# Optimization experiments

Measured on AMD Instinct MI355X. Metric: run time of the kernel, lower is better.

The kernel has to match this reference:

```python
import jax, jax.numpy as jnp
import numpy as np

SIM_TIME = 3
ALPHA = 0.9      # membrane decay
RHO = 0.985      # threshold-adaptation decay
BETA_A = 1.8     # adaptation coupling
TH = 1.0         # base threshold
SURR_SCALE = 0.3 # surrogate gradient scale

@jax.custom_vjp
def spike(v):
    return (v > 0.0).astype(v.dtype)

def _spike_fwd(v):
    return spike(v), v

def _spike_bwd(v, g):
    # triangular surrogate gradient
    return (g * SURR_SCALE * jnp.maximum(0.0, 1.0 - jnp.abs(v)),)

spike.defvjp(_spike_fwd, _spike_bwd)

def setup_inputs() -> dict:
    key = jax.random.key(0)
    ks = jax.random.split(key, 6)
    T, B, nin, npre, nad, npost, nout = 32, 128, 512, 1024, 1024, 1024, 256
    s = lambda fan_in: 1.0 / np.sqrt(fan_in)
    return {
        "inp": jax.random.normal(ks[0], (T, B, nin), dtype=jnp.float32),
        "W_pre": jax.random.normal(ks[1], (npre, nin + nad), dtype=jnp.float32) * s(nin + nad),
        "b_pre": jnp.zeros((npre,), jnp.float32),
        "W_ad": jax.random.normal(ks[2], (nad, npre), dtype=jnp.float32) * s(npre),
        "b_ad": jnp.zeros((nad,), jnp.float32),
        "W_post": jax.random.normal(ks[3], (npost, nin + nad), dtype=jnp.float32) * s(nin + nad),
        "b_post": jnp.zeros((npost,), jnp.float32),
        "W_out": jax.random.normal(ks[4], (nout, npost), dtype=jnp.float32) * s(npost),
        "b_out": jnp.zeros((nout,), jnp.float32),
    }

def _rsnn_forward(inp, W_pre, b_pre, W_ad, b_ad, W_post, b_post, W_out, b_out):
    T, B, _ = inp.shape
    nad = W_ad.shape[0]
    npre = W_pre.shape[0]
    npost = W_post.shape[0]
    z = lambda n: jnp.zeros((B, n), inp.dtype)
    # state: (adaptive spikes, v_pre, v_adapt, b_adapt, v_post)
    init = (z(nad), z(npre), z(nad), z(nad), z(npost))

    def step_t(state, inp_t):
        spikes, v_pre, v_a, b_a, v_post = state
        o = None
        for _ in range(SIM_TIME):  # fixed small inner simulation loop
            x = jnp.concatenate([inp_t, spikes], axis=1)            # [B, nin+nad]
            v_pre = ALPHA * v_pre + x @ W_pre.T + b_pre
            s_pre = spike(v_pre - TH)
            v_pre = v_pre - s_pre * TH                               # soft reset
            v_a = ALPHA * v_a + s_pre @ W_ad.T + b_ad
            th_eff = TH + BETA_A * b_a                               # adaptive threshold
            s_a = spike(v_a - th_eff)
            v_a = v_a - s_a * th_eff
            b_a = RHO * b_a + s_a
            spikes = s_a
            x2 = jnp.concatenate([inp_t, s_a], axis=1)
            v_post = ALPHA * v_post + x2 @ W_post.T + b_post
            s_post = spike(v_post - TH)
            v_post = v_post - s_post * TH
            o = s_post @ W_out.T + b_out                             # [B, nout]
        return (spikes, v_pre, v_a, b_a, v_post), o

    final_state, output = jax.lax.scan(step_t, init, inp)            # output [T, B, nout]
    return output, final_state[0]

def reference(inp, W_pre, b_pre, W_ad, b_ad, W_post, b_post, W_out, b_out):
    return _rsnn_forward(inp, W_pre, b_pre, W_ad, b_ad, W_post, b_post, W_out, b_out)
```

## Files before the change

kernel.cpp:

```cpp
#include <hip/hip_runtime.h>

#pragma clang fp contract(off)

typedef unsigned long long u64;
typedef unsigned int u32;

#define ALPHA  0.9f
#define RHO    0.985f
#define BETA_A 1.8f
#define TH     1.0f
#define CAP    (1 << 24)

__global__ __launch_bounds__(256) void transpose_k(const float* __restrict__ src,
                                                   float* __restrict__ dst,
                                                   int R, int C) {
    __shared__ float tile[32][33];
    const int c0 = blockIdx.x * 32;
    const int r0 = blockIdx.y * 32;
    const int tx = threadIdx.x, ty = threadIdx.y;
#pragma unroll
    for (int i = 0; i < 4; ++i)
        tile[ty + i * 8][tx] = src[(r0 + ty + i * 8) * C + c0 + tx];
    __syncthreads();
#pragma unroll
    for (int i = 0; i < 4; ++i)
        dst[(c0 + ty + i * 8) * R + r0 + tx] = tile[tx][ty + i * 8];
}

__global__ __launch_bounds__(256) void ip_gemm2(const float* __restrict__ inp,
                                                const float* __restrict__ Wt_a,
                                                const float* __restrict__ bias_a,
                                                float* __restrict__ out_a,
                                                const float* __restrict__ Wt_b,
                                                const float* __restrict__ bias_b,
                                                float* __restrict__ out_b) {
    __shared__ __align__(16) float s_in[512 * 20];
    const int tid   = threadIdx.x;
    const int chunk = blockIdx.x;
    const int rbase = blockIdx.y * 16;

    for (int idx = tid; idx < 16 * 512; idx += 256) {
        const int r = idx >> 9, k = idx & 511;
        s_in[k * 20 + r] = inp[(rbase + r) * 512 + k];
    }
    __syncthreads();

    const int n = chunk * 256 + tid;
    float acca[16], accb[16];
#pragma unroll
    for (int r = 0; r < 16; ++r) { acca[r] = 0.f; accb[r] = 0.f; }

    for (int k = 0; k < 512; ++k) {
        const float wa = Wt_a[k * 1024 + n];
        const float wb = Wt_b[k * 1024 + n];
        const float4* p = (const float4*)(s_in + k * 20);
        const float4 x0 = p[0], x1 = p[1], x2 = p[2], x3 = p[3];
        acca[0]  = fmaf(x0.x, wa, acca[0]);  accb[0]  = fmaf(x0.x, wb, accb[0]);
        acca[1]  = fmaf(x0.y, wa, acca[1]);  accb[1]  = fmaf(x0.y, wb, accb[1]);
        acca[2]  = fmaf(x0.z, wa, acca[2]);  accb[2]  = fmaf(x0.z, wb, accb[2]);
        acca[3]  = fmaf(x0.w, wa, acca[3]);  accb[3]  = fmaf(x0.w, wb, accb[3]);
        acca[4]  = fmaf(x1.x, wa, acca[4]);  accb[4]  = fmaf(x1.x, wb, accb[4]);
        acca[5]  = fmaf(x1.y, wa, acca[5]);  accb[5]  = fmaf(x1.y, wb, accb[5]);
        acca[6]  = fmaf(x1.z, wa, acca[6]);  accb[6]  = fmaf(x1.z, wb, accb[6]);
        acca[7]  = fmaf(x1.w, wa, acca[7]);  accb[7]  = fmaf(x1.w, wb, accb[7]);
        acca[8]  = fmaf(x2.x, wa, acca[8]);  accb[8]  = fmaf(x2.x, wb, accb[8]);
        acca[9]  = fmaf(x2.y, wa, acca[9]);  accb[9]  = fmaf(x2.y, wb, accb[9]);
        acca[10] = fmaf(x2.z, wa, acca[10]); accb[10] = fmaf(x2.z, wb, accb[10]);
        acca[11] = fmaf(x2.w, wa, acca[11]); accb[11] = fmaf(x2.w, wb, accb[11]);
        acca[12] = fmaf(x3.x, wa, acca[12]); accb[12] = fmaf(x3.x, wb, accb[12]);
        acca[13] = fmaf(x3.y, wa, acca[13]); accb[13] = fmaf(x3.y, wb, accb[13]);
        acca[14] = fmaf(x3.z, wa, acca[14]); accb[14] = fmaf(x3.z, wb, accb[14]);
        acca[15] = fmaf(x3.w, wa, acca[15]); accb[15] = fmaf(x3.w, wb, accb[15]);
    }
    const float bna = bias_a[n];
    const float bnb = bias_b[n];
#pragma unroll
    for (int r = 0; r < 16; ++r) {
        out_a[(rbase + r) * 1024 + n] = acca[r] + bna;
        out_b[(rbase + r) * 1024 + n] = accb[r] + bnb;
    }
}

__device__ __forceinline__ u64 ld_u64(const u64* p) {
    return __hip_atomic_load(p, __ATOMIC_RELAXED, __HIP_MEMORY_SCOPE_AGENT);
}
__device__ __forceinline__ void st_u64(u64* p, u64 v) {
    __hip_atomic_store(p, v, __ATOMIC_RELAXED, __HIP_MEMORY_SCOPE_AGENT);
}
__device__ __forceinline__ u64 ld_lds(const u64* p) {
    return __hip_atomic_load(p, __ATOMIC_RELAXED, __HIP_MEMORY_SCOPE_WORKGROUP);
}
__device__ __forceinline__ void st_lds(u64* p, u64 v) {
    __hip_atomic_store(p, v, __ATOMIC_RELAXED, __HIP_MEMORY_SCOPE_WORKGROUP);
}
__device__ __forceinline__ int ld_seq(const int* p) {
    return __hip_atomic_load(p, __ATOMIC_ACQUIRE, __HIP_MEMORY_SCOPE_WORKGROUP);
}
__device__ __forceinline__ void st_seq(int* p, int v) {
    __hip_atomic_store(p, v, __ATOMIC_RELEASE, __HIP_MEMORY_SCOPE_WORKGROUP);
}

__device__ __forceinline__ float gatherseg(const char* __restrict__ Wb,
                                           const int* __restrict__ list,
                                           int i0, int i1, int colB) {
    float a0 = 0.f, a1 = 0.f, a2 = 0.f, a3 = 0.f;
    int i = i0;
    for (; i + 4 <= i1; i += 4) {
        const int4 j = *(const int4*)(list + i);
        a0 += *(const float*)(Wb + (u32)(j.x + colB));
        a1 += *(const float*)(Wb + (u32)(j.y + colB));
        a2 += *(const float*)(Wb + (u32)(j.z + colB));
        a3 += *(const float*)(Wb + (u32)(j.w + colB));
    }
    for (; i < i1; ++i) a0 += *(const float*)(Wb + (u32)(list[i] + colB));
    return (a0 + a1) + (a2 + a3);
}

__device__ __forceinline__ void gather2seg(const char* __restrict__ Wc,
                                           const char* __restrict__ Wa,
                                           const int* __restrict__ list,
                                           int cnt, int colB,
                                           float& accC, float& accA) {
    float c0 = 0.f, c1 = 0.f, c2 = 0.f, c3 = 0.f;
    float a0 = 0.f, a1 = 0.f, a2 = 0.f, a3 = 0.f;
    int i = 0;
    for (; i + 4 <= cnt; i += 4) {
        const int4 j = *(const int4*)(list + i);
        c0 += *(const float*)(Wc + (u32)(j.x + colB));
        a0 += *(const float*)(Wa + (u32)(j.x + colB));
        c1 += *(const float*)(Wc + (u32)(j.y + colB));
        a1 += *(const float*)(Wa + (u32)(j.y + colB));
        c2 += *(const float*)(Wc + (u32)(j.z + colB));
        a2 += *(const float*)(Wa + (u32)(j.z + colB));
        c3 += *(const float*)(Wc + (u32)(j.w + colB));
        a3 += *(const float*)(Wa + (u32)(j.w + colB));
    }
    for (; i < cnt; ++i) {
        const u32 off = (u32)(list[i] + colB);
        c0 += *(const float*)(Wc + off);
        a0 += *(const float*)(Wa + off);
    }
    accC = (c0 + c1) + (c2 + c3);
    accA = (a0 + a1) + (a2 + a3);
}

__device__ __forceinline__ float gather_idx(const float* __restrict__ W,
                                            const int* __restrict__ list, int cnt, int col) {
    float a0 = 0.f, a1 = 0.f, a2 = 0.f, a3 = 0.f;
    int i = 0;
    for (; i + 4 <= cnt; i += 4) {
        const int4 j = *(const int4*)(list + i);
        a0 += W[j.x * 256 + col];
        a1 += W[j.y * 256 + col];
        a2 += W[j.z * 256 + col];
        a3 += W[j.w * 256 + col];
    }
    for (; i < cnt; ++i) a0 += W[list[i] * 256 + col];
    return (a0 + a1) + (a2 + a3);
}

__global__ __launch_bounds__(640) void rsnn_nb(
    const float* __restrict__ Wt_pre,
    const float* __restrict__ Wt_ad,
    const float* __restrict__ Wt_post,
    const float* __restrict__ IP_pre,
    const float* __restrict__ IP_post,
    const float* __restrict__ b_ad_p,
    u64* __restrict__ lines,
    u64* __restrict__ spkO,
    float* __restrict__ out)
{
    const int tid  = threadIdx.x;
    const int bid  = blockIdx.x;
    const int x    = bid & 7;
    const int g    = bid >> 3;
    const int s    = x >> 1;
    const int p    = g * 2 + (x & 1);
    const int wid  = tid >> 6;
    const int lane = tid & 63;
    const u64 M32  = 0xffffffffull;

    __shared__ __align__(16) int listP[2][1024];
    __shared__ __align__(16) int listS[2][1024];
    __shared__ u64 ltag[2][2][2][8];
    __shared__ int seqP[2], seqS[2], cntP[2], cntS[2];

    if (tid < 64) ((u64*)ltag)[tid] = 0;
    if (tid < 2) { seqP[tid] = 0; seqS[tid] = 0; }
    __syncthreads();

    const char* WadB    = (const char*)Wt_ad;
    const char* WpreAB  = (const char*)(Wt_pre  + 512 * 1024);
    const char* WpostAB = (const char*)(Wt_post + 512 * 1024);

    if (wid < 8) {
        const int bi   = wid >> 2;
        const int q    = wid & 3;
        const int b    = 2 * p + bi;
        const int col  = s * 256 + q * 64 + lane;
        const int colB = col * 4;

        float v_pre = 0.f, v_a = 0.f, ba = 0.f, v_post = 0.f, accA = 0.f;
        bool  sa = false;
        const float bad = b_ad_p[col];
        float ipre = 0.f, ipost = 0.f;

        for (int e = 1; e <= 96; ++e) {
            const int par = e & 1;
            const u64 tag = ((u64)e) << 32;
            if ((e - 1) % 3 == 0) {
                const int t = (e - 1) / 3;
                ipre  = IP_pre [(t * 128 + b) * 1024 + col];
                ipost = IP_post[(t * 128 + b) * 1024 + col];
            }
            u64* gl0 = lines + ((b * 2 + par) * 2 + 0) * 32;
            u64* gl1 = lines + ((b * 2 + par) * 2 + 1) * 32;

            v_pre = ALPHA * v_pre + ipre + accA;
            float d = v_pre - TH;
            const bool sp = d > 0.f;
            if (sp) v_pre = d;
            {
                const u64 m = __ballot(sp);
                if (lane == 0) {
                    st_u64(&gl0[s * 8 + 2 * q],     tag | (m & M32));
                    st_u64(&gl0[s * 8 + 2 * q + 1], tag | (m >> 32));
                    st_lds(&ltag[bi][par][0][2 * q],     tag | (m & M32));
                    st_lds(&ltag[bi][par][0][2 * q + 1], tag | (m >> 32));
                }
            }
            {
                int gd = 0;
                while (ld_seq(&seqP[bi]) < e && ++gd < CAP) {}
            }
            const float accB = gatherseg(WadB, listP[bi], 0, cntP[bi], colB);
            v_a = ALPHA * v_a + accB + bad;
            const float th = TH + BETA_A * ba;
            d = v_a - th;
            sa = d > 0.f;
            if (sa) v_a = d;
            ba = RHO * ba + (sa ? 1.f : 0.f);
            {
                const u64 m = __ballot(sa);
                if (lane == 0) {
                    st_u64(&gl1[s * 8 + 2 * q],     tag | (m & M32));
                    st_u64(&gl1[s * 8 + 2 * q + 1], tag | (m >> 32));
                    st_lds(&ltag[bi][par][1][2 * q],     tag | (m & M32));
                    st_lds(&ltag[bi][par][1][2 * q + 1], tag | (m >> 32));
                }
            }
            {
                int gd = 0;
                while (ld_seq(&seqS[bi]) < e && ++gd < CAP) {}
            }
            float accC;
            gather2seg(WpostAB, WpreAB, listS[bi], cntS[bi], colB, accC, accA);
            v_post = ALPHA * v_post + ipost + accC;
            d = v_post - TH;
            const bool spost = d > 0.f;
            if (spost) v_post = d;
            if (e % 3 == 0) {
                const u64 m = __ballot(spost);
                if (lane == 0)
                    st_u64(&spkO[(((e - 1) / 3) * 128 + b) * 16 + s * 4 + q], m);
            }
            if (e == 96)
                out[32 * 128 * 256 + b * 1024 + col] = sa ? 1.f : 0.f;
        }
    } else {
        const int bi = wid - 8;
        const int b  = 2 * p + bi;
        const bool act = lane < 32;
        const int sl = lane >> 3, h = lane & 7;
        const int jbase = (sl * 256 + h * 32) << 12;

        for (int e = 1; e <= 96; ++e) {
            const int par = e & 1;
            const u64* gl0 = lines + ((b * 2 + par) * 2 + 0) * 32;
            const u64* gl1 = lines + ((b * 2 + par) * 2 + 1) * 32;

            u32 bits = 0;
            if (act) {
                u64 v; int gd = 0;
                if (sl == s) {
                    do { v = ld_lds(&ltag[bi][par][0][h]); }
                    while ((v >> 32) != (u64)e && ++gd < CAP);
                } else {
                    do { v = ld_u64(&gl0[lane]); }
                    while ((v >> 32) != (u64)e && ++gd < CAP);
                }
                bits = (u32)v;
            }
            {
                const int pc = __popc(bits);
                int incl = pc;
#pragma unroll
                for (int dlt = 1; dlt < 32; dlt <<= 1) {
                    const int v = __shfl_up(incl, dlt, 64);
                    if (lane >= dlt && lane < 32) incl += v;
                }
                int base = incl - pc;
                u32 m = bits;
                while (m) {
                    const int bt = __builtin_ctz(m);
                    m &= m - 1;
                    listP[bi][base++] = jbase + (bt << 12);
                }
                if (lane == 31) { cntP[bi] = incl; st_seq(&seqP[bi], e); }
            }

            bits = 0;
            if (act) {
                u64 v; int gd = 0;
                if (sl == s) {
                    do { v = ld_lds(&ltag[bi][par][1][h]); }
                    while ((v >> 32) != (u64)e && ++gd < CAP);
                } else {
                    do { v = ld_u64(&gl1[lane]); }
                    while ((v >> 32) != (u64)e && ++gd < CAP);
                }
                bits = (u32)v;
            }
            {
                const int pc = __popc(bits);
                int incl = pc;
#pragma unroll
                for (int dlt = 1; dlt < 32; dlt <<= 1) {
                    const int v = __shfl_up(incl, dlt, 64);
                    if (lane >= dlt && lane < 32) incl += v;
                }
                int base = incl - pc;
                u32 m = bits;
                while (m) {
                    const int bt = __builtin_ctz(m);
                    m &= m - 1;
                    listS[bi][base++] = jbase + (bt << 12);
                }
                if (lane == 31) { cntS[bi] = incl; st_seq(&seqS[bi], e); }
            }
        }
    }
}

__global__ __launch_bounds__(256) void out_gemm(const float* __restrict__ Wt_out,
                                                const float* __restrict__ b_out,
                                                const u64* __restrict__ spkO,
                                                float* __restrict__ out) {
    __shared__ u64 bmp[16];
    __shared__ int pc[16];
    __shared__ __align__(16) int list[1024];
    const int r = blockIdx.x, tid = threadIdx.x;
    if (tid < 16) {
        const u64 m = ld_u64(&spkO[r * 16 + tid]);
        bmp[tid] = m;
        pc[tid]  = __popcll(m);
    }
    __syncthreads();
    int total = 0;
#pragma unroll
    for (int w = 0; w < 16; ++w) total += pc[w];
    for (int j = tid; j < 1024; j += 256) {
        const int w = j >> 6, bit = j & 63;
        const u64 m = bmp[w];
        if ((m >> bit) & 1ull) {
            int base = __popcll(m & ((1ull << bit) - 1ull));
            for (int q2 = 0; q2 < w; ++q2) base += pc[q2];
            list[base] = j;
        }
    }
    __syncthreads();
    const float acc = gather_idx(Wt_out, list, total, tid);
    out[r * 256 + tid] = acc + b_out[tid];
}

extern "C" void kernel_launch(void* const* d_in, const int* in_sizes, int n_in,
                              void* d_out, int out_size, void* d_ws, size_t ws_size,
                              hipStream_t stream) {
    (void)in_sizes; (void)n_in; (void)out_size; (void)ws_size;
    const float* inp    = (const float*)d_in[0];
    const float* W_pre  = (const float*)d_in[1];
    const float* b_pre  = (const float*)d_in[2];
    const float* W_ad   = (const float*)d_in[3];
    const float* b_ad   = (const float*)d_in[4];
    const float* W_post = (const float*)d_in[5];
    const float* b_post = (const float*)d_in[6];
    const float* W_out  = (const float*)d_in[7];
    const float* b_out  = (const float*)d_in[8];

    char* base = (char*)d_ws;
    u64*  lines = (u64*)(base + 4096);
    u64*  spkO  = (u64*)(base + 4096 + 131072);
    float* ws      = (float*)(base + 1048576);
    float* Wt_pre  = ws;
    float* Wt_post = Wt_pre  + 1536 * 1024;
    float* Wt_ad   = Wt_post + 1536 * 1024;
    float* Wt_out  = Wt_ad   + 1024 * 1024;
    float* IP_pre  = Wt_out  + 1024 * 256;
    float* IP_post = IP_pre  + 4096 * 1024;

    hipMemsetAsync(base, 0, 4096 + 131072, stream);

    transpose_k<<<dim3(48, 32), dim3(32, 8), 0, stream>>>(W_pre,  Wt_pre,  1024, 1536);
    transpose_k<<<dim3(48, 32), dim3(32, 8), 0, stream>>>(W_post, Wt_post, 1024, 1536);
    transpose_k<<<dim3(32, 32), dim3(32, 8), 0, stream>>>(W_ad,   Wt_ad,   1024, 1024);
    transpose_k<<<dim3(32, 8),  dim3(32, 8), 0, stream>>>(W_out,  Wt_out,  256,  1024);

    ip_gemm2<<<dim3(4, 256), 256, 0, stream>>>(inp, Wt_pre, b_pre, IP_pre,
                                               Wt_post, b_post, IP_post);

    rsnn_nb<<<256, 640, 0, stream>>>(Wt_pre, Wt_ad, Wt_post,
                                     IP_pre, IP_post, b_ad,
                                     lines, spkO, (float*)d_out);

    out_gemm<<<4096, 256, 0, stream>>>(Wt_out, b_out, spkO, (float*)d_out);
}
```

Before: 1.067 ms.

## Regroup blocks to four batches per block and defer post-layer gather to overlap waits

Each block now handles 4 batch rows with 128 columns per slice (8 slices) instead of 2 rows with 256 columns, so there are 8 compute waves plus 4 list-builder waves per block. The post-layer gather for step e-1 is split in two halves and moved into the spin-wait windows of step e, using double-buffered spike lists. The pre-layer recurrent gather is separated and done right after the adaptive spike list is ready. The aim is to hide the synchronization latency between the compute and list-building waves behind useful gather work. The cost is more shared memory for the double buffers, a longer per-step critical path, and an extra tail step for the final post update.

```diff
diff --git a/kernel.cpp b/kernel.cpp
--- a/kernel.cpp
+++ b/kernel.cpp
@@ -116,34 +116,6 @@
     return (a0 + a1) + (a2 + a3);
 }
 
-__device__ __forceinline__ void gather2seg(const char* __restrict__ Wc,
-                                           const char* __restrict__ Wa,
-                                           const int* __restrict__ list,
-                                           int cnt, int colB,
-                                           float& accC, float& accA) {
-    float c0 = 0.f, c1 = 0.f, c2 = 0.f, c3 = 0.f;
-    float a0 = 0.f, a1 = 0.f, a2 = 0.f, a3 = 0.f;
-    int i = 0;
-    for (; i + 4 <= cnt; i += 4) {
-        const int4 j = *(const int4*)(list + i);
-        c0 += *(const float*)(Wc + (u32)(j.x + colB));
-        a0 += *(const float*)(Wa + (u32)(j.x + colB));
-        c1 += *(const float*)(Wc + (u32)(j.y + colB));
-        a1 += *(const float*)(Wa + (u32)(j.y + colB));
-        c2 += *(const float*)(Wc + (u32)(j.z + colB));
-        a2 += *(const float*)(Wa + (u32)(j.z + colB));
-        c3 += *(const float*)(Wc + (u32)(j.w + colB));
-        a3 += *(const float*)(Wa + (u32)(j.w + colB));
-    }
-    for (; i < cnt; ++i) {
-        const u32 off = (u32)(list[i] + colB);
-        c0 += *(const float*)(Wc + off);
-        a0 += *(const float*)(Wa + off);
-    }
-    accC = (c0 + c1) + (c2 + c3);
-    accA = (a0 + a1) + (a2 + a3);
-}
-
 __device__ __forceinline__ float gather_idx(const float* __restrict__ W,
                                             const int* __restrict__ list, int cnt, int col) {
     float a0 = 0.f, a1 = 0.f, a2 = 0.f, a3 = 0.f;
@@ -159,7 +131,7 @@
     return (a0 + a1) + (a2 + a3);
 }
 
-__global__ __launch_bounds__(640) void rsnn_nb(
+__global__ __launch_bounds__(768) void rsnn_nb4(
     const float* __restrict__ Wt_pre,
     const float* __restrict__ Wt_ad,
     const float* __restrict__ Wt_post,
@@ -172,21 +144,19 @@
 {
     const int tid  = threadIdx.x;
     const int bid  = blockIdx.x;
-    const int x    = bid & 7;
+    const int s    = bid & 7;
     const int g    = bid >> 3;
-    const int s    = x >> 1;
-    const int p    = g * 2 + (x & 1);
     const int wid  = tid >> 6;
     const int lane = tid & 63;
     const u64 M32  = 0xffffffffull;
 
-    __shared__ __align__(16) int listP[2][1024];
-    __shared__ __align__(16) int listS[2][1024];
-    __shared__ u64 ltag[2][2][2][8];
-    __shared__ int seqP[2], seqS[2], cntP[2], cntS[2];
+    __shared__ __align__(16) int listP[4][1024];
+    __shared__ __align__(16) int listS[2][4][1024];
+    __shared__ u64 ltag[4][2][2][4];
+    __shared__ int seqP[4], seqS[4], cntP[4], cntS[4];
 
     if (tid < 64) ((u64*)ltag)[tid] = 0;
-    if (tid < 2) { seqP[tid] = 0; seqS[tid] = 0; }
+    if (tid < 4) { seqP[tid] = 0; seqS[tid] = 0; }
     __syncthreads();
 
     const char* WadB    = (const char*)Wt_ad;
@@ -194,25 +164,23 @@
     const char* WpostAB = (const char*)(Wt_post + 512 * 1024);
 
     if (wid < 8) {
-        const int bi   = wid >> 2;
-        const int q    = wid & 3;
-        const int b    = 2 * p + bi;
-        const int col  = s * 256 + q * 64 + lane;
+        const int bi   = wid >> 1;
+        const int h    = wid & 1;
+        const int b    = 4 * g + bi;
+        const int col  = s * 128 + h * 64 + lane;
         const int colB = col * 4;
 
         float v_pre = 0.f, v_a = 0.f, ba = 0.f, v_post = 0.f, accA = 0.f;
         bool  sa = false;
         const float bad = b_ad_p[col];
-        float ipre = 0.f, ipost = 0.f;
+        float ipre = 0.f, g1 = 0.f;
+        int halfPrev = 0, cntPrev = 0, parPrev = 0;
 
         for (int e = 1; e <= 96; ++e) {
             const int par = e & 1;
             const u64 tag = ((u64)e) << 32;
-            if ((e - 1) % 3 == 0) {
-                const int t = (e - 1) / 3;
-                ipre  = IP_pre [(t * 128 + b) * 1024 + col];
-                ipost = IP_post[(t * 128 + b) * 1024 + col];
-            }
+            if ((e - 1) % 3 == 0)
+                ipre = IP_pre[(((e - 1) / 3) * 128 + b) * 1024 + col];
             u64* gl0 = lines + ((b * 2 + par) * 2 + 0) * 32;
             u64* gl1 = lines + ((b * 2 + par) * 2 + 1) * 32;
 
@@ -223,16 +191,16 @@
             {
                 const u64 m = __ballot(sp);
                 if (lane == 0) {
-                    st_u64(&gl0[s * 8 + 2 * q],     tag | (m & M32));
-                    st_u64(&gl0[s * 8 + 2 * q + 1], tag | (m >> 32));
-                    st_lds(&ltag[bi][par][0][2 * q],     tag | (m & M32));
-                    st_lds(&ltag[bi][par][0][2 * q + 1], tag | (m >> 32));
-                }
-            }
-            {
-                int gd = 0;
-                while (ld_seq(&seqP[bi]) < e && ++gd < CAP) {}
-            }
+                    st_u64(&gl0[s * 4 + h * 2],     tag | (m & M32));
+                    st_u64(&gl0[s * 4 + h * 2 + 1], tag | (m >> 32));
+                    st_lds(&ltag[bi][par][0][h * 2],     tag | (m & M32));
+                    st_lds(&ltag[bi][par][0][h * 2 + 1], tag | (m >> 32));
+                }
+            }
+            if (e >= 2)
+                g1 = gatherseg(WpostAB, listS[parPrev][bi], 0, halfPrev, colB);
+            { int gd = 0; while (ld_seq(&seqP[bi]) < e && ++gd < CAP) {} }
+
             const float accB = gatherseg(WadB, listP[bi], 0, cntP[bi], colB);
             v_a = ALPHA * v_a + accB + bad;
             const float th = TH + BETA_A * ba;
@@ -243,36 +211,55 @@
             {
                 const u64 m = __ballot(sa);
                 if (lane == 0) {
-                    st_u64(&gl1[s * 8 + 2 * q],     tag | (m & M32));
-                    st_u64(&gl1[s * 8 + 2 * q + 1], tag | (m >> 32));
-                    st_lds(&ltag[bi][par][1][2 * q],     tag | (m & M32));
-                    st_lds(&ltag[bi][par][1][2 * q + 1], tag | (m >> 32));
-                }
-            }
-            {
-                int gd = 0;
-                while (ld_seq(&seqS[bi]) < e && ++gd < CAP) {}
-            }
-            float accC;
-            gather2seg(WpostAB, WpreAB, listS[bi], cntS[bi], colB, accC, accA);
-            v_post = ALPHA * v_post + ipost + accC;
-            d = v_post - TH;
-            const bool spost = d > 0.f;
-            if (spost) v_post = d;
-            if (e % 3 == 0) {
-                const u64 m = __ballot(spost);
-                if (lane == 0)
-                    st_u64(&spkO[(((e - 1) / 3) * 128 + b) * 16 + s * 4 + q], m);
+                    st_u64(&gl1[s * 4 + h * 2],     tag | (m & M32));
+                    st_u64(&gl1[s * 4 + h * 2 + 1], tag | (m >> 32));
+                    st_lds(&ltag[bi][par][1][h * 2],     tag | (m & M32));
+                    st_lds(&ltag[bi][par][1][h * 2 + 1], tag | (m >> 32));
+                }
+            }
+            if (e >= 2) {
+                const float g2 = gatherseg(WpostAB, listS[parPrev][bi],
+                                           halfPrev, cntPrev, colB);
+                const int tp = (e - 2) / 3;
+                const float ipost = IP_post[(tp * 128 + b) * 1024 + col];
+                v_post = ALPHA * v_post + ipost + (g1 + g2);
+                float dd = v_post - TH;
+                const bool spost = dd > 0.f;
+                if (spost) v_post = dd;
+                if (e % 3 == 1) {
+                    const u64 m = __ballot(spost);
+                    if (lane == 0)
+                        st_u64(&spkO[(tp * 128 + b) * 16 + s * 2 + h], m);
+                }
             }
             if (e == 96)
                 out[32 * 128 * 256 + b * 1024 + col] = sa ? 1.f : 0.f;
+            { int gd = 0; while (ld_seq(&seqS[bi]) < e && ++gd < CAP) {} }
+
+            const int cs = cntS[bi];
+            if (e < 96)
+                accA = gatherseg(WpreAB, listS[par][bi], 0, cs, colB);
+            halfPrev = (cs >> 1) & ~3;
+            cntPrev  = cs;
+            parPrev  = par;
+        }
+        {
+            const float ga = gatherseg(WpostAB, listS[0][bi], 0, halfPrev, colB);
+            const float gb = gatherseg(WpostAB, listS[0][bi], halfPrev, cntPrev, colB);
+            const float ipost = IP_post[(31 * 128 + b) * 1024 + col];
+            v_post = ALPHA * v_post + ipost + (ga + gb);
+            const float dd = v_post - TH;
+            const u64 m = __ballot(dd > 0.f);
+            if (lane == 0)
+                st_u64(&spkO[(31 * 128 + b) * 16 + s * 2 + h], m);
         }
     } else {
-        const int bi = wid - 8;
-        const int b  = 2 * p + bi;
+        const int bi  = wid - 8;
+        const int b   = 4 * g + bi;
         const bool act = lane < 32;
-        const int sl = lane >> 3, h = lane & 7;
-        const int jbase = (sl * 256 + h * 32) << 12;
+        const int w   = lane;
+        const int jbase = w << 17;
+        const bool own  = (w >> 2) == s;
 
         for (int e = 1; e <= 96; ++e) {
             const int par = e & 1;
@@ -282,11 +269,11 @@
             u32 bits = 0;
             if (act) {
                 u64 v; int gd = 0;
-                if (sl == s) {
-                    do { v = ld_lds(&ltag[bi][par][0][h]); }
+                if (own) {
+                    do { v = ld_lds(&ltag[bi][par][0][w & 3]); }
                     while ((v >> 32) != (u64)e && ++gd < CAP);
                 } else {
-                    do { v = ld_u64(&gl0[lane]); }
+                    do { v = ld_u64(&gl0[w]); }
                     while ((v >> 32) != (u64)e && ++gd < CAP);
                 }
                 bits = (u32)v;
@@ -312,11 +299,11 @@
             bits = 0;
             if (act) {
                 u64 v; int gd = 0;
-                if (sl == s) {
-                    do { v = ld_lds(&ltag[bi][par][1][h]); }
+                if (own) {
+                    do { v = ld_lds(&ltag[bi][par][1][w & 3]); }
                     while ((v >> 32) != (u64)e && ++gd < CAP);
                 } else {
-                    do { v = ld_u64(&gl1[lane]); }
+                    do { v = ld_u64(&gl1[w]); }
                     while ((v >> 32) != (u64)e && ++gd < CAP);
                 }
                 bits = (u32)v;
@@ -334,7 +321,7 @@
                 while (m) {
                     const int bt = __builtin_ctz(m);
                     m &= m - 1;
-                    listS[bi][base++] = jbase + (bt << 12);
+                    listS[par][bi][base++] = jbase + (bt << 12);
                 }
                 if (lane == 31) { cntS[bi] = incl; st_seq(&seqS[bi], e); }
             }
@@ -408,9 +395,9 @@
     ip_gemm2<<<dim3(4, 256), 256, 0, stream>>>(inp, Wt_pre, b_pre, IP_pre,
                                                Wt_post, b_post, IP_post);
 
-    rsnn_nb<<<256, 640, 0, stream>>>(Wt_pre, Wt_ad, Wt_post,
-                                     IP_pre, IP_post, b_ad,
-                                     lines, spkO, (float*)d_out);
+    rsnn_nb4<<<256, 768, 0, stream>>>(Wt_pre, Wt_ad, Wt_post,
+                                      IP_pre, IP_post, b_ad,
+                                      lines, spkO, (float*)d_out);
 
     out_gemm<<<4096, 256, 0, stream>>>(Wt_out, b_out, spkO, (float*)d_out);
 }
```

Result: slower. 1.251 ms (+17.2%).
